# Kernel optimization log

Hardware: AMD Instinct MI355X
Metric: run time of the kernel (lower is better)

Reference implementation:

```python
import jax, jax.numpy as jnp
import numpy as np

B, T, S = 16, 128, 128          # batch, temporal, spatial (road segments)
NIN, SIN = 3, 1                 # number / speed input feature sizes
NH, SH, DH = 64, 64, 128        # number-enc / speed-enc / decoder hidden
T_PREDICT = 20


def _p(k, shape, scale=0.05):
    return (jax.random.normal(k, shape) * scale).astype(jnp.float32)


def setup_inputs() -> dict:
    key = jax.random.key(0)
    ks = jax.random.split(key, 16)
    inp = {"input_data": jax.random.normal(ks[0], (B, T, S, NIN + SIN), dtype=jnp.float32)}
    # seg_model cells: LSTM gates driven by input x, own hidden h, spatial neighbors h_after/h_before
    inp.update(
        n_Wx=_p(ks[1], (NIN, 4 * NH)), n_Wh=_p(ks[2], (NH, 4 * NH)),
        n_Wa=_p(ks[3], (NH, 4 * NH)), n_Wb=_p(ks[4], (NH, 4 * NH)),
        n_b=jnp.zeros((4 * NH,), jnp.float32),
        s_Wx=_p(ks[5], (SIN, 4 * SH)), s_Wh=_p(ks[6], (SH, 4 * SH)),
        s_Wa=_p(ks[7], (SH, 4 * SH)), s_Wb=_p(ks[8], (SH, 4 * SH)),
        s_b=jnp.zeros((4 * SH,), jnp.float32),
        d_Wx=_p(ks[9], (NH + SH, 4 * DH)), d_Wh=_p(ks[10], (DH, 4 * DH)),
        d_Wa=_p(ks[11], (DH, 4 * DH)), d_Wb=_p(ks[12], (DH, 4 * DH)),
        d_b=jnp.zeros((4 * DH,), jnp.float32),
        on_W=_p(ks[13], (DH, 1)), on_b=jnp.zeros((1,), jnp.float32),
        os_W=_p(ks[14], (DH, 1)), os_b=jnp.zeros((1,), jnp.float32),
    )
    return inp


def _cell(x, h, c, ha, hb, Wx, Wh, Wa, Wb, b):
    g = x @ Wx + h @ Wh + ha @ Wa + hb @ Wb + b
    i, f, u, o = jnp.split(g, 4, axis=-1)
    c2 = jax.nn.sigmoid(f) * c + jax.nn.sigmoid(i) * jnp.tanh(u)
    return jax.nn.sigmoid(o) * jnp.tanh(c2), c2


def _shift(h):
    # h_after[s] = h[s+1], h_before[s] = h[s-1], zero-padded at the boundary
    z = jnp.zeros_like(h[:, :1])
    return jnp.concatenate([h[:, 1:], z], axis=1), jnp.concatenate([z, h[:, :-1]], axis=1)


def _next_input(former_number, next_x, output):
    # output: [B,S,2] = (number_out, speed_out)
    speed_in = next_x[:, :1, 3:]                                    # [B,1,1]
    speed_next = jnp.concatenate([speed_in, output[:, 1:, 1:]], axis=1)
    inflow = jnp.concatenate([next_x[:, 0:1, 1:2], output[:, :-1, 0:1]], axis=1)
    number_calc = former_number[:, :, 2:3] + inflow - output[:, :, 0:1]
    return jnp.concatenate([output[:, :, 0:1], inflow, number_calc, speed_next], axis=2)


def reference(input_data, n_Wx, n_Wh, n_Wa, n_Wb, n_b,
              s_Wx, s_Wh, s_Wa, s_Wb, s_b,
              d_Wx, d_Wh, d_Wa, d_Wb, d_b,
              on_W, on_b, os_W, os_b):
    b, t, s, _ = input_data.shape
    zeros = lambda hdim: jnp.zeros((b, s, hdim), input_data.dtype)
    init = (zeros(NH), zeros(NH), zeros(SH), zeros(SH), zeros(DH), zeros(DH))

    def step(carry, xs):
        hn, cn, hs, cs, hd, cd = carry
        x_t, x_tp1 = xs
        hn_a, hn_b = _shift(hn)
        hs_a, hs_b = _shift(hs)
        hd_a, hd_b = _shift(hd)
        num = x_t[:, :, :NIN]
        spd = x_t[:, :, NIN:]
        hn, cn = _cell(num, hn, cn, hn_a, hn_b, n_Wx, n_Wh, n_Wa, n_Wb, n_b)
        hs, cs = _cell(spd, hs, cs, hs_a, hs_b, s_Wx, s_Wh, s_Wa, s_Wb, s_b)
        dec_in = jnp.concatenate([hn, hs], axis=2)
        hd, cd = _cell(dec_in, hd, cd, hd_a, hd_b, d_Wx, d_Wh, d_Wa, d_Wb, d_b)
        output = jnp.concatenate([hd @ on_W + on_b, hd @ os_W + os_b], axis=2)
        data = _next_input(num, x_tp1, output)
        return (hn, cn, hs, cs, hd, cd), data

    xs = (jnp.moveaxis(input_data[:, :-1], 1, 0),   # x_t,   t = 0..T-2 (time-major)
          jnp.moveaxis(input_data[:, 1:], 1, 0))    # x_{t+1}
    _, datas = jax.lax.scan(step, init, xs)          # [T-1, B, S, 4]
    # original writes outputs only for time >= t_predict; slicing is equivalent
    return jnp.moveaxis(datas[T_PREDICT:], 0, 1)     # [B, T-T_PREDICT-1, S, 4]
```

## Files before the change

kernel.cpp:

```cpp
#include <hip/hip_runtime.h>

constexpr int B_ = 16, T_ = 128, S_ = 128;
constexpr int ROWS = B_ * S_;
constexpr int NSTEPS = T_ - 1;
constexpr int TPRED = 20;
constexpr int TOUT = NSTEPS - TPRED;
constexpr int TB = 512;
constexpr int NBLK = 160;

constexpr int OFF_HN = 0;
constexpr int OFF_HS = OFF_HN + 262144;
constexpr int OFF_HD = OFF_HS + 262144;
constexpr int OFF_BAR = OFF_HD + 262144;
constexpr int OFF_OUTS = OFF_BAR + 8192;
constexpr int OFF_NPK = OFF_OUTS + NSTEPS * ROWS * 2;
constexpr int NPK_DW = 16 * 7 * 256;
constexpr int OFF_SPK = OFF_NPK + NPK_DW;
constexpr int OFF_DPK = OFF_SPK + NPK_DW;
constexpr int DPK_DW = 32 * 16 * 256;
constexpr int PACK_DWORDS = 2 * NPK_DW + DPK_DW;
constexpr int ZERO_DW = OFF_NPK;

typedef _Float16 half8 __attribute__((ext_vector_type(8)));
typedef float float4v __attribute__((ext_vector_type(4)));
typedef unsigned long long ull;

__device__ __forceinline__ float sigm(float x) { return 1.f / (1.f + __expf(-x)); }
__device__ __forceinline__ float tanh_(float x) { return 2.f / (1.f + __expf(-2.f * x)) - 1.f; }
__device__ __forceinline__ unsigned int pack2(float a, float b) {
    union { unsigned int u; _Float16 h[2]; } x;
    x.h[0] = (_Float16)a; x.h[1] = (_Float16)b; return x.u;
}

__device__ __forceinline__ unsigned ld_dev_u32(const unsigned* p) {
    return __hip_atomic_load(p, __ATOMIC_RELAXED, __HIP_MEMORY_SCOPE_AGENT);
}
__device__ __forceinline__ ull ld_dev_u64(const ull* p) {
    return __hip_atomic_load(p, __ATOMIC_RELAXED, __HIP_MEMORY_SCOPE_AGENT);
}
__device__ __forceinline__ void st_dev_u64(ull* p, ull v) {
    __hip_atomic_store(p, v, __ATOMIC_RELAXED, __HIP_MEMORY_SCOPE_AGENT);
}
__device__ __forceinline__ void at_add_u32(unsigned* p, unsigned v) {
    __hip_atomic_fetch_add(p, v, __ATOMIC_RELAXED, __HIP_MEMORY_SCOPE_AGENT);
}
__device__ __forceinline__ void at_add_f32(float* p, float v) {
    __hip_atomic_fetch_add(p, v, __ATOMIC_RELAXED, __HIP_MEMORY_SCOPE_AGENT);
}
#define WAIT_VM0() asm volatile("s_waitcnt vmcnt(0)" ::: "memory")

__global__ __launch_bounds__(256) void pack_weights(
    const float* __restrict__ nWx, const float* __restrict__ nWh,
    const float* __restrict__ nWa, const float* __restrict__ nWb, const float* __restrict__ nb,
    const float* __restrict__ sWx, const float* __restrict__ sWh,
    const float* __restrict__ sWa, const float* __restrict__ sWb, const float* __restrict__ sb,
    const float* __restrict__ dWx, const float* __restrict__ dWh,
    const float* __restrict__ dWa, const float* __restrict__ dWb,
    unsigned int* __restrict__ wsu)
{
    int idx = blockIdx.x * 256 + threadIdx.x;
    if (idx >= PACK_DWORDS) return;
    if (idx < 2 * NPK_DW) {
        bool isS = idx >= NPK_DW;
        int dn = isS ? idx - NPK_DW : idx;
        int tile = dn >> 8;
        int e = (dn & 255) * 2;
        int lane = e >> 3, j0 = e & 7;
        int quad = lane >> 4;
        int nt = tile / 7, tt = tile % 7;
        int col = nt * 16 + (lane & 15);
        float v0, v1;
        if (tt < 6) {
            const float* W = isS ? ((tt < 2) ? sWh : (tt < 4) ? sWa : sWb)
                                 : ((tt < 2) ? nWh : (tt < 4) ? nWa : nWb);
            int k = (tt & 1) * 32 + quad * 8 + j0;
            v0 = W[k * 256 + col]; v1 = W[(k + 1) * 256 + col];
        } else {
            int kl = quad * 8 + j0;
            auto xv = [&](int k) -> float {
                if (!isS) { if (k < 3) return nWx[k * 256 + col]; if (k == 3) return nb[col]; return 0.f; }
                else      { if (k == 4) return sWx[col]; if (k == 5) return sb[col]; return 0.f; }
            };
            v0 = xv(kl); v1 = xv(kl + 1);
        }
        wsu[(isS ? OFF_SPK : OFF_NPK) + dn] = pack2(v0, v1);
    } else {
        int dd = idx - 2 * NPK_DW;
        int tile = dd >> 8;
        int e = (dd & 255) * 2;
        int lane = e >> 3, j0 = e & 7;
        int quad = lane >> 4;
        int nt = tile >> 4, tt = tile & 15;
        const float* W = (tt < 4) ? dWx : (tt < 8) ? dWh : (tt < 12) ? dWa : dWb;
        int k = (tt & 3) * 32 + quad * 8 + j0;
        int col = nt * 16 + (lane & 15);
        wsu[OFF_DPK + dd] = pack2(W[k * 512 + col], W[(k + 1) * 512 + col]);
    }
}

__global__ __launch_bounds__(TB) void pipe_persist(
    const float* __restrict__ input,
    const float* __restrict__ db,
    const float* __restrict__ onW, const float* __restrict__ onb,
    const float* __restrict__ osW, const float* __restrict__ osb,
    float* __restrict__ ws)
{
    const int tid = threadIdx.x;
    const int wave = tid >> 6, lane = tid & 63;
    const int quad = lane >> 4, l15 = lane & 15;
    const int blk = blockIdx.x;

    unsigned* wsu = (unsigned*)ws;
    char* hnB = (char*)(wsu + OFF_HN);
    char* hsB = (char*)(wsu + OFF_HS);
    char* hdB = (char*)(wsu + OFF_HD);
    unsigned* nsc = wsu + OFF_BAR;
    unsigned* dc  = wsu + OFF_BAR + 1024;
    float* outs = ws + OFF_OUTS;

    union SMem {
        struct {
            _Float16 pk[16 * 7 * 512];
            _Float16 hst[2][130][72];
            _Float16 xa[128][40];
        } ns;
        struct {
            _Float16 wd[4 * 16 * 512];
            _Float16 dec[128][136];
            _Float16 hd[130][136];
            _Float16 hpub[128][16];
        } d;
    };
    __shared__ __align__(16) SMem sm;

    if (blk < 32) {
        const bool isS = (blk >= 16);
        const int rg = blk & 15;
        char* hB = isS ? hsB : hnB;
        unsigned* dcp = dc + rg * 32;
        unsigned* nscp = nsc + rg * 32;

        const ull* pkG = (const ull*)(wsu + (isS ? OFF_SPK : OFF_NPK));
        for (int i = tid; i < 14336; i += TB) ((ull*)sm.ns.pk)[i] = pkG[i];
        for (int i = tid; i < 9360; i += TB) ((unsigned*)sm.ns.hst)[i] = 0u;
        for (int i = tid; i < 2560; i += TB) ((unsigned*)sm.ns.xa)[i] = 0u;
        float4v c4[4];
#pragma unroll
        for (int cg = 0; cg < 4; ++cg) c4[cg] = (float4v){0.f, 0.f, 0.f, 0.f};
        __syncthreads();

        for (int e = 0; e < NSTEPS; ++e) {
            const int pinL = (e + 1) & 1, poutL = e & 1;
            const int poutG = e & 3;
            if (tid < 128) {
                const float* xp = input + ((size_t)(rg * T_ + e) * S_ + tid) * 4;
                unsigned* row = (unsigned*)sm.ns.xa + tid * 20;
                row[0] = pack2(xp[0], xp[1]);
                row[1] = pack2(xp[2], 1.f);
                row[2] = pack2(xp[3], 1.f);
            }
            if (e >= 4) {
                unsigned tgt = 8u * (unsigned)(e - 3);
                while (ld_dev_u32(dcp) < tgt) __builtin_amdgcn_s_sleep(1);
            }
            __syncthreads();

            const _Float16* hb = &sm.ns.hst[pinL][0][0];
            const int ri = wave * 16 + l15;
            half8 ah0 = *(const half8*)(hb + (ri + 1) * 72 + quad * 8);
            half8 ah1 = *(const half8*)(hb + (ri + 1) * 72 + 32 + quad * 8);
            half8 aa0 = *(const half8*)(hb + (ri + 2) * 72 + quad * 8);
            half8 aa1 = *(const half8*)(hb + (ri + 2) * 72 + 32 + quad * 8);
            half8 ab0 = *(const half8*)(hb + (ri) * 72 + quad * 8);
            half8 ab1 = *(const half8*)(hb + (ri) * 72 + 32 + quad * 8);
            half8 ax  = *(const half8*)(&sm.ns.xa[0][0] + ri * 40 + quad * 8);
            _Float16* hLp = &sm.ns.hst[poutL][0][0];
#pragma unroll
            for (int cg = 0; cg < 4; ++cg) {
                float4v acc[4];
#pragma unroll
                for (int g = 0; g < 4; ++g) acc[g] = (float4v){0.f, 0.f, 0.f, 0.f};
#pragma unroll
                for (int g = 0; g < 4; ++g) {
                    const _Float16* base = sm.ns.pk + (size_t)(4 * g + cg) * 7 * 512 + lane * 8;
                    acc[g] = __builtin_amdgcn_mfma_f32_16x16x32_f16(ah0, *(const half8*)(base),        acc[g], 0, 0, 0);
                    acc[g] = __builtin_amdgcn_mfma_f32_16x16x32_f16(ah1, *(const half8*)(base + 512),  acc[g], 0, 0, 0);
                    acc[g] = __builtin_amdgcn_mfma_f32_16x16x32_f16(aa0, *(const half8*)(base + 1024), acc[g], 0, 0, 0);
                    acc[g] = __builtin_amdgcn_mfma_f32_16x16x32_f16(aa1, *(const half8*)(base + 1536), acc[g], 0, 0, 0);
                    acc[g] = __builtin_amdgcn_mfma_f32_16x16x32_f16(ab0, *(const half8*)(base + 2048), acc[g], 0, 0, 0);
                    acc[g] = __builtin_amdgcn_mfma_f32_16x16x32_f16(ab1, *(const half8*)(base + 2560), acc[g], 0, 0, 0);
                    acc[g] = __builtin_amdgcn_mfma_f32_16x16x32_f16(ax,  *(const half8*)(base + 3072), acc[g], 0, 0, 0);
                }
                const int kcol = cg * 16 + l15;
                float4v cold = c4[cg], cnew;
#pragma unroll
                for (int r = 0; r < 4; ++r) {
                    float c2 = sigm(acc[1][r]) * cold[r] + sigm(acc[0][r]) * tanh_(acc[2][r]);
                    float h2 = sigm(acc[3][r]) * tanh_(c2);
                    cnew[r] = c2;
                    int row = wave * 16 + quad * 4 + r;
                    hLp[(row + 1) * 72 + kcol] = (_Float16)h2;
                }
                c4[cg] = cnew;
            }
            __syncthreads();
            {
                char* dst0 = hB + (size_t)poutG * 262144 + (size_t)rg * 16384;
#pragma unroll
                for (int k = 0; k < 4; ++k) {
                    int i = tid + k * 512;
                    int row = i >> 4, j = i & 15;
                    ull v = *((const ull*)&sm.ns.hst[poutL][row + 1][0] + j);
                    st_dev_u64((ull*)(dst0 + (size_t)row * 128 + (size_t)j * 8), v);
                }
            }
            WAIT_VM0();
            __syncthreads();
            if (tid == 0) at_add_u32(nscp, 1u);
        }
    } else {
        const int idx = blk - 32;
        const int rg = idx >> 3;
        const int c = idx & 7;
        const int r0 = rg * 128;
        unsigned* dcp = dc + rg * 32;
        unsigned* nscp = nsc + rg * 32;

        const ull* pdG = (const ull*)(wsu + OFF_DPK);
        for (int i = tid; i < 8192; i += TB) {
            int tile = i >> 7, j = i & 127;
            int g = tile >> 4, tt = tile & 15;
            ((ull*)sm.d.wd)[(g * 16 + tt) * 128 + j] =
                pdG[(size_t)((g * 8 + c) * 16 + tt) * 128 + j];
        }
        if (tid < 68) {
            ((unsigned*)&sm.d.hd[0][0])[tid] = 0u;
            ((unsigned*)&sm.d.hd[129][0])[tid] = 0u;
        }
        const int hcol = c * 16 + l15;
        const float won = onW[hcol], wos = osW[hcol];
        float bg[4];
#pragma unroll
        for (int g = 0; g < 4; ++g) bg[g] = db[g * 128 + hcol];
        float4v creg = (float4v){0.f, 0.f, 0.f, 0.f};
        __syncthreads();

        for (int e = 1; e <= NSTEPS; ++e) {
            const int t = e - 1;
            const int pdec = t & 3;
            const int phdin = e & 1;
            const int phdout = t & 1;
            {
                unsigned tgt = 2u * (unsigned)e;
                while (ld_dev_u32(nscp) < tgt) __builtin_amdgcn_s_sleep(1);
            }
            {
                ull t8[8];
#pragma unroll
                for (int k = 0; k < 8; ++k) {
                    int i = tid + k * 512;
                    int row = i >> 5, j = i & 31;
                    const char* src = (j < 16 ? hnB : hsB) + (size_t)pdec * 262144
                                      + (size_t)(r0 + row) * 128 + (size_t)(j & 15) * 8;
                    t8[k] = ld_dev_u64((const ull*)src);
                }
#pragma unroll
                for (int k = 0; k < 8; ++k) {
                    int i = tid + k * 512;
                    int row = i >> 5, j = i & 31;
                    *((ull*)&sm.d.dec[row][0] + j) = t8[k];
                }
            }
            if (e >= 2) {
                unsigned tgt = 8u * (unsigned)(e - 1);
                while (ld_dev_u32(dcp) < tgt) __builtin_amdgcn_s_sleep(1);
            }
            {
                ull t8[8];
#pragma unroll
                for (int k = 0; k < 8; ++k) {
                    int i = tid + k * 512;
                    int row = i >> 5, j = i & 31;
                    t8[k] = ld_dev_u64((const ull*)(hdB + (size_t)phdin * 524288
                                       + (size_t)(r0 + row) * 256 + (size_t)j * 8));
                }
#pragma unroll
                for (int k = 0; k < 8; ++k) {
                    int i = tid + k * 512;
                    int row = i >> 5, j = i & 31;
                    *((ull*)&sm.d.hd[row + 1][0] + j) = t8[k];
                }
            }
            __syncthreads();

            const int ri = wave * 16 + l15;
            half8 fr[16];
#pragma unroll
            for (int kt = 0; kt < 4; ++kt) {
                fr[kt]      = *(const half8*)(&sm.d.dec[ri][0] + kt * 32 + quad * 8);
                fr[4 + kt]  = *(const half8*)(&sm.d.hd[ri + 1][0] + kt * 32 + quad * 8);
                fr[8 + kt]  = *(const half8*)(&sm.d.hd[ri + 2][0] + kt * 32 + quad * 8);
                fr[12 + kt] = *(const half8*)(&sm.d.hd[ri][0] + kt * 32 + quad * 8);
            }
            float4v acc[4];
#pragma unroll
            for (int g = 0; g < 4; ++g) acc[g] = (float4v){0.f, 0.f, 0.f, 0.f};
#pragma unroll
            for (int g = 0; g < 4; ++g) {
                const _Float16* bw = sm.d.wd + (size_t)(g * 16) * 512 + lane * 8;
#pragma unroll
                for (int kt = 0; kt < 16; ++kt)
                    acc[g] = __builtin_amdgcn_mfma_f32_16x16x32_f16(fr[kt], *(const half8*)(bw + kt * 512), acc[g], 0, 0, 0);
            }
            float4v cold = creg, cnew;
            float h2s[4];
#pragma unroll
            for (int r = 0; r < 4; ++r) {
                float c2 = sigm(acc[1][r] + bg[1]) * cold[r] + sigm(acc[0][r] + bg[0]) * tanh_(acc[2][r] + bg[2]);
                float h2 = sigm(acc[3][r] + bg[3]) * tanh_(c2);
                cnew[r] = c2;
                h2s[r] = h2;
                int row = wave * 16 + quad * 4 + r;
                sm.d.hpub[row][l15] = (_Float16)h2;
            }
            creg = cnew;
            __syncthreads();
            {
                int prow = tid >> 2, jj = tid & 3;
                ull v = *((const ull*)&sm.d.hpub[prow][0] + jj);
                st_dev_u64((ull*)(hdB + (size_t)phdout * 524288 + (size_t)(r0 + prow) * 256
                           + (size_t)c * 32 + (size_t)jj * 8), v);
            }
            WAIT_VM0();
            __syncthreads();
            if (tid == 0) at_add_u32(dcp, 1u);
#pragma unroll
            for (int r = 0; r < 4; ++r) {
                int row = wave * 16 + quad * 4 + r;
                float pon = h2s[r] * won, pos = h2s[r] * wos;
#pragma unroll
                for (int off = 8; off; off >>= 1) {
                    pon += __shfl_down(pon, off, 16);
                    pos += __shfl_down(pos, off, 16);
                }
                if (l15 == 0) {
                    float* o = outs + ((size_t)t * ROWS + (r0 + row)) * 2;
                    at_add_f32(o, pon);
                    at_add_f32(o + 1, pos);
                }
            }
        }
    }
}

__global__ __launch_bounds__(256) void assemble_kernel(
    const float* __restrict__ input, const float* __restrict__ ws, float* __restrict__ out,
    const float* __restrict__ onb, const float* __restrict__ osb)
{
    const float* outs = ws + OFF_OUTS;
    int idx = blockIdx.x * 256 + threadIdx.x;
    if (idx >= B_ * TOUT * S_) return;
    float b_on = onb[0], b_os = osb[0];
    int s = idx & 127;
    int tmp = idx >> 7;
    int tt = tmp % TOUT;
    int b = tmp / TOUT;
    int t = tt + TPRED;
    int row = b * S_ + s;
    float o0 = outs[((size_t)t * ROWS + row) * 2 + 0] + b_on;
    float o1 = outs[((size_t)t * ROWS + row) * 2 + 1] + b_os;
    float inflow = (s == 0) ? input[(((size_t)b * T_ + (t + 1)) * S_ + 0) * 4 + 1]
                            : (outs[((size_t)t * ROWS + row - 1) * 2 + 0] + b_on);
    float numc = input[(((size_t)b * T_ + t) * S_ + s) * 4 + 2] + inflow - o0;
    float spd = (s == 0) ? input[(((size_t)b * T_ + (t + 1)) * S_ + 0) * 4 + 3] : o1;
    float4 v = make_float4(o0, inflow, numc, spd);
    reinterpret_cast<float4*>(out)[idx] = v;
}

extern "C" void kernel_launch(void* const* d_in, const int* in_sizes, int n_in,
                              void* d_out, int out_size, void* d_ws, size_t ws_size,
                              hipStream_t stream) {
    const float* input = (const float*)d_in[0];
    const float* nWx = (const float*)d_in[1];
    const float* nWh = (const float*)d_in[2];
    const float* nWa = (const float*)d_in[3];
    const float* nWb = (const float*)d_in[4];
    const float* nb  = (const float*)d_in[5];
    const float* sWx = (const float*)d_in[6];
    const float* sWh = (const float*)d_in[7];
    const float* sWa = (const float*)d_in[8];
    const float* sWb = (const float*)d_in[9];
    const float* sb  = (const float*)d_in[10];
    const float* dWx = (const float*)d_in[11];
    const float* dWh = (const float*)d_in[12];
    const float* dWa = (const float*)d_in[13];
    const float* dWb = (const float*)d_in[14];
    const float* db  = (const float*)d_in[15];
    const float* onW = (const float*)d_in[16];
    const float* onb = (const float*)d_in[17];
    const float* osW = (const float*)d_in[18];
    const float* osb = (const float*)d_in[19];

    float* ws = (float*)d_ws;

    hipMemsetAsync(ws, 0, (size_t)ZERO_DW * 4, stream);

    pack_weights<<<dim3((PACK_DWORDS + 255) / 256), dim3(256), 0, stream>>>(
        nWx, nWh, nWa, nWb, nb, sWx, sWh, sWa, sWb, sb,
        dWx, dWh, dWa, dWb, (unsigned int*)ws);

    void* kargs[] = {
        (void*)&input, (void*)&db, (void*)&onW, (void*)&onb,
        (void*)&osW, (void*)&osb, (void*)&ws
    };
    hipLaunchCooperativeKernel((void*)pipe_persist, dim3(NBLK), dim3(TB),
                               kargs, 0, stream);

    int nout = B_ * TOUT * S_;
    assemble_kernel<<<dim3((nout + 255) / 256), dim3(256), 0, stream>>>(
        input, ws, (float*)d_out, onb, osb);
}
```

Before: 1.186 ms.

## Repartition decoder blocks by row chunks with neighbor-only halo exchange

The decoder blocks now each own 16 consecutive spatial rows and all 128 hidden columns (8 waves × 16 columns), rather than 128 rows × 16 columns. Each block keeps its own decoder hidden state in LDS and exchanges only the boundary rows with its two neighbouring blocks through per-block progress flags. This removes the per-step full 128x128 hidden-state global round trip and the wait on all 8 column blocks. In exchange, weights are no longer staged in LDS and are read from global memory (L2) by every MFMA each step, which may add load latency.

```diff
diff --git a/kernel.cpp b/kernel.cpp
--- a/kernel.cpp
+++ b/kernel.cpp
@@ -39,6 +39,9 @@
     return __hip_atomic_load(p, __ATOMIC_RELAXED, __HIP_MEMORY_SCOPE_AGENT);
 }
 __device__ __forceinline__ void st_dev_u64(ull* p, ull v) {
+    __hip_atomic_store(p, v, __ATOMIC_RELAXED, __HIP_MEMORY_SCOPE_AGENT);
+}
+__device__ __forceinline__ void st_dev_u32(unsigned* p, unsigned v) {
     __hip_atomic_store(p, v, __ATOMIC_RELAXED, __HIP_MEMORY_SCOPE_AGENT);
 }
 __device__ __forceinline__ void at_add_u32(unsigned* p, unsigned v) {
@@ -116,7 +119,9 @@
     char* hdB = (char*)(wsu + OFF_HD);
     unsigned* nsc = wsu + OFF_BAR;
     unsigned* dc  = wsu + OFF_BAR + 1024;
+    unsigned* dpr = wsu + OFF_BAR + 2048;
     float* outs = ws + OFF_OUTS;
+    const _Float16* pd = (const _Float16*)((const unsigned*)ws + OFF_DPK);
 
     union SMem {
         struct {
@@ -125,10 +130,8 @@
             _Float16 xa[128][40];
         } ns;
         struct {
-            _Float16 wd[4 * 16 * 512];
-            _Float16 dec[128][136];
-            _Float16 hd[130][136];
-            _Float16 hpub[128][16];
+            _Float16 dec[16][136];
+            _Float16 hdl[2][18][136];
         } d;
     };
     __shared__ __align__(16) SMem sm;
@@ -221,23 +224,19 @@
     } else {
         const int idx = blk - 32;
         const int rg = idx >> 3;
-        const int c = idx & 7;
-        const int r0 = rg * 128;
+        const int r0 = idx * 16;
+        const bool leftOK = (idx & 7) != 0;
+        const bool rightOK = (idx & 7) != 7;
         unsigned* dcp = dc + rg * 32;
         unsigned* nscp = nsc + rg * 32;
-
-        const ull* pdG = (const ull*)(wsu + OFF_DPK);
-        for (int i = tid; i < 8192; i += TB) {
-            int tile = i >> 7, j = i & 127;
-            int g = tile >> 4, tt = tile & 15;
-            ((ull*)sm.d.wd)[(g * 16 + tt) * 128 + j] =
-                pdG[(size_t)((g * 8 + c) * 16 + tt) * 128 + j];
-        }
-        if (tid < 68) {
-            ((unsigned*)&sm.d.hd[0][0])[tid] = 0u;
-            ((unsigned*)&sm.d.hd[129][0])[tid] = 0u;
-        }
-        const int hcol = c * 16 + l15;
+        unsigned* myp = dpr + idx * 32;
+        unsigned* lp = dpr + (leftOK ? (idx - 1) : idx) * 32;
+        unsigned* rp = dpr + (rightOK ? (idx + 1) : idx) * 32;
+
+        for (int i = tid; i < 1088; i += TB) ((unsigned*)sm.d.dec)[i] = 0u;
+        for (int i = tid; i < 2448; i += TB) ((unsigned*)sm.d.hdl)[i] = 0u;
+
+        const int hcol = wave * 16 + l15;
         const float won = onW[hcol], wos = osW[hcol];
         float bg[4];
 #pragma unroll
@@ -248,95 +247,86 @@
         for (int e = 1; e <= NSTEPS; ++e) {
             const int t = e - 1;
             const int pdec = t & 3;
-            const int phdin = e & 1;
-            const int phdout = t & 1;
+            const int pin = e & 1;
+            const int pout = (e + 1) & 1;
             {
                 unsigned tgt = 2u * (unsigned)e;
                 while (ld_dev_u32(nscp) < tgt) __builtin_amdgcn_s_sleep(1);
             }
             {
-                ull t8[8];
-#pragma unroll
-                for (int k = 0; k < 8; ++k) {
-                    int i = tid + k * 512;
-                    int row = i >> 5, j = i & 31;
-                    const char* src = (j < 16 ? hnB : hsB) + (size_t)pdec * 262144
-                                      + (size_t)(r0 + row) * 128 + (size_t)(j & 15) * 8;
-                    t8[k] = ld_dev_u64((const ull*)src);
-                }
-#pragma unroll
-                for (int k = 0; k < 8; ++k) {
-                    int i = tid + k * 512;
-                    int row = i >> 5, j = i & 31;
-                    *((ull*)&sm.d.dec[row][0] + j) = t8[k];
-                }
+                int row = tid >> 5, j = tid & 31;
+                int hf = j >> 4, jj = j & 15;
+                const char* src = (hf ? hsB : hnB) + (size_t)pdec * 262144
+                                  + (size_t)(r0 + row) * 128 + (size_t)jj * 8;
+                ull v = ld_dev_u64((const ull*)src);
+                *((ull*)&sm.d.dec[row][hf * 64] + jj) = v;
             }
             if (e >= 2) {
-                unsigned tgt = 8u * (unsigned)(e - 1);
-                while (ld_dev_u32(dcp) < tgt) __builtin_amdgcn_s_sleep(1);
-            }
-            {
-                ull t8[8];
-#pragma unroll
-                for (int k = 0; k < 8; ++k) {
-                    int i = tid + k * 512;
-                    int row = i >> 5, j = i & 31;
-                    t8[k] = ld_dev_u64((const ull*)(hdB + (size_t)phdin * 524288
-                                       + (size_t)(r0 + row) * 256 + (size_t)j * 8));
-                }
-#pragma unroll
-                for (int k = 0; k < 8; ++k) {
-                    int i = tid + k * 512;
-                    int row = i >> 5, j = i & 31;
-                    *((ull*)&sm.d.hd[row + 1][0] + j) = t8[k];
-                }
-            }
-            __syncthreads();
-
-            const int ri = wave * 16 + l15;
+                unsigned tgt = (unsigned)(e - 1);
+                if (tid == 0 && leftOK)
+                    while (ld_dev_u32(lp) < tgt) __builtin_amdgcn_s_sleep(1);
+                if (tid == 64 && rightOK)
+                    while (ld_dev_u32(rp) < tgt) __builtin_amdgcn_s_sleep(1);
+            }
+            __syncthreads();
+            if (tid < 64) {
+                int side = tid >> 5, j = tid & 31;
+                bool valid = side ? rightOK : leftOK;
+                int grow = side ? (r0 + 16) : (r0 - 1);
+                ull v = 0;
+                if (valid)
+                    v = ld_dev_u64((const ull*)(hdB + (size_t)pin * 524288
+                                                + (size_t)grow * 256) + j);
+                *((ull*)&sm.d.hdl[pin][side ? 17 : 0][0] + j) = v;
+            }
+            __syncthreads();
+
+            const _Float16* hdp = &sm.d.hdl[pin][0][0];
             half8 fr[16];
 #pragma unroll
             for (int kt = 0; kt < 4; ++kt) {
-                fr[kt]      = *(const half8*)(&sm.d.dec[ri][0] + kt * 32 + quad * 8);
-                fr[4 + kt]  = *(const half8*)(&sm.d.hd[ri + 1][0] + kt * 32 + quad * 8);
-                fr[8 + kt]  = *(const half8*)(&sm.d.hd[ri + 2][0] + kt * 32 + quad * 8);
-                fr[12 + kt] = *(const half8*)(&sm.d.hd[ri][0] + kt * 32 + quad * 8);
+                fr[kt]      = *(const half8*)(&sm.d.dec[l15][0] + kt * 32 + quad * 8);
+                fr[4 + kt]  = *(const half8*)(hdp + (l15 + 1) * 136 + kt * 32 + quad * 8);
+                fr[8 + kt]  = *(const half8*)(hdp + (l15 + 2) * 136 + kt * 32 + quad * 8);
+                fr[12 + kt] = *(const half8*)(hdp + (l15) * 136 + kt * 32 + quad * 8);
             }
             float4v acc[4];
 #pragma unroll
             for (int g = 0; g < 4; ++g) acc[g] = (float4v){0.f, 0.f, 0.f, 0.f};
 #pragma unroll
             for (int g = 0; g < 4; ++g) {
-                const _Float16* bw = sm.d.wd + (size_t)(g * 16) * 512 + lane * 8;
+                const _Float16* bw = pd + (size_t)((g * 8 + wave) * 16) * 512 + lane * 8;
 #pragma unroll
                 for (int kt = 0; kt < 16; ++kt)
                     acc[g] = __builtin_amdgcn_mfma_f32_16x16x32_f16(fr[kt], *(const half8*)(bw + kt * 512), acc[g], 0, 0, 0);
             }
             float4v cold = creg, cnew;
             float h2s[4];
+            _Float16* ho = &sm.d.hdl[pout][0][0];
 #pragma unroll
             for (int r = 0; r < 4; ++r) {
                 float c2 = sigm(acc[1][r] + bg[1]) * cold[r] + sigm(acc[0][r] + bg[0]) * tanh_(acc[2][r] + bg[2]);
                 float h2 = sigm(acc[3][r] + bg[3]) * tanh_(c2);
                 cnew[r] = c2;
                 h2s[r] = h2;
-                int row = wave * 16 + quad * 4 + r;
-                sm.d.hpub[row][l15] = (_Float16)h2;
+                int row = quad * 4 + r;
+                ho[(row + 1) * 136 + hcol] = (_Float16)h2;
             }
             creg = cnew;
             __syncthreads();
-            {
-                int prow = tid >> 2, jj = tid & 3;
-                ull v = *((const ull*)&sm.d.hpub[prow][0] + jj);
-                st_dev_u64((ull*)(hdB + (size_t)phdout * 524288 + (size_t)(r0 + prow) * 256
-                           + (size_t)c * 32 + (size_t)jj * 8), v);
+            if (tid < 64) {
+                int side = tid >> 5, j = tid & 31;
+                ull v = *((const ull*)&sm.d.hdl[pout][side ? 16 : 1][0] + j);
+                st_dev_u64((ull*)(hdB + (size_t)pout * 524288
+                                  + (size_t)(r0 + (side ? 15 : 0)) * 256) + j, v);
             }
             WAIT_VM0();
             __syncthreads();
             if (tid == 0) at_add_u32(dcp, 1u);
+            if (tid == 64) st_dev_u32(myp, (unsigned)e);
 #pragma unroll
             for (int r = 0; r < 4; ++r) {
-                int row = wave * 16 + quad * 4 + r;
+                int row = quad * 4 + r;
                 float pon = h2s[r] * won, pos = h2s[r] * wos;
 #pragma unroll
                 for (int off = 8; off; off >>= 1) {
```

Result: slower. 1.447 ms (+22.0%).
